# Kernel tuning notes

Measured on AMD Instinct MI355X. Metric: run time of the kernel, lower is better.

## Reference

```python
import jax, jax.numpy as jnp
import numpy as np

NLAT = 192  # octahedral O96-class grid


def _lons(nlat):
    half = [20 + 4 * i for i in range(nlat // 2)]
    return half + half[::-1]


def _dft_matrix(nlat, mmax):
    # Truncated per-ring real-DFT basis (torch.fft.rfft convention, 'forward' 1/n norm).
    # Ring j has nlon_j points; frequencies beyond its Nyquist (m > nlon_j//2) are zero.
    lons = _lons(nlat)
    max_nlon = max(lons)
    D = np.zeros((nlat, max_nlon, mmax), dtype=np.complex64)
    for j, n in enumerate(lons):
        keep = min(mmax, n // 2 + 1)
        k = np.arange(n)[:, None]
        m = np.arange(keep)[None, :]
        D[j, :n, :keep] = np.exp(-2j * np.pi * k * m / n) / n
    return D


def _legendre_weights(nlat, lmax, mmax):
    # Orthonormalized associated Legendre P_l^m at Gaussian latitudes (north->south),
    # with Gaussian quadrature weights and the 2*pi longitude factor folded in.
    xg, wg = np.polynomial.legendre.leggauss(nlat)
    x = xg[::-1].copy()
    w = wg[::-1].copy()
    s = np.sqrt(1.0 - x * x)
    leg = np.zeros((lmax, mmax, nlat))
    pmm = np.full(nlat, 1.0 / np.sqrt(4.0 * np.pi))
    for m in range(mmax):
        if m > 0:
            pmm = -np.sqrt((2 * m + 1) / (2.0 * m)) * s * pmm
        if m < lmax:
            leg[m, m] = pmm
        if m + 1 < lmax:
            leg[m + 1, m] = np.sqrt(2 * m + 3.0) * x * pmm
        for l in range(m + 2, lmax):
            a = np.sqrt((4.0 * l * l - 1.0) / (l * l - m * m))
            bb = np.sqrt(((2.0 * l + 1.0) * (l - 1 + m) * (l - 1 - m)) / ((2.0 * l - 3.0) * (l * l - m * m)))
            leg[l, m] = a * x * leg[l - 1, m] - bb * leg[l - 2, m]
    leg = 2.0 * np.pi * leg * w[None, None, :]
    return leg.astype(np.float32)


def setup_inputs() -> dict:
    key = jax.random.key(0)
    nlat = NLAT
    lmax = mmax = nlat // 2
    n_points = sum(_lons(nlat))  # 40320 for nlat=192
    data = jax.random.normal(key, (4, 1, 1, n_points, 100), dtype=jnp.float32)
    dft = jnp.asarray(_dft_matrix(nlat, mmax))
    leg = jnp.asarray(_legendre_weights(nlat, lmax, mmax))
    return {"data": data, "dft": dft, "leg": leg}


def reference(data, dft, leg):
    b, t, e, p, v = data.shape
    nlat, max_nlon, mmax = dft.shape
    lmax = leg.shape[0]
    lons = _lons(nlat)
    # static scatter map: flattened ragged rings -> [nlat, max_nlon] padded layout
    flat_idx = np.concatenate([j * max_nlon + np.arange(n) for j, n in enumerate(lons)])
    x = jnp.transpose(data, (0, 1, 2, 4, 3)).reshape(-1, p)  # [(b t e v), p]
    B = x.shape[0]
    x_pad = jnp.zeros((B, nlat * max_nlon), x.dtype).at[:, flat_idx].set(x)
    x_pad = x_pad.reshape(B, nlat, max_nlon)
    # ragged per-ring truncated real DFT, then associated-Legendre contraction
    f_hat = jnp.einsum('bjn,jnm->bjm', x_pad, dft)        # [B, nlat, mmax] complex
    coeffs = jnp.einsum('bjm,lmj->blm', f_hat, leg)       # [B, lmax, mmax] complex
    coeffs = coeffs.reshape(b, t, e, v, lmax, mmax)
    return jnp.transpose(coeffs, (0, 1, 2, 4, 5, 3))      # [b, t, e, yF, xF, v]
```

## Files before the change

### kernel.cpp

```cpp
#include <hip/hip_runtime.h>

#define NLAT 192
#define NPTS 40320
#define MMAX 96
#define LMAX 96
#define NV   100
#define MAXN 400
#define NB   400

typedef __attribute__((ext_vector_type(8))) _Float16 half8v;
typedef __attribute__((ext_vector_type(4))) float f32x4;

#define FSTR 40

static __device__ __forceinline__ float bits2f(unsigned int b) {
    union { unsigned int i; float f; } v; v.i = b; return v.f;
}
static __device__ __forceinline__ unsigned int f2bf(float f) {
    union { float f; unsigned int i; } v; v.f = f;
    return (v.i + 0x7FFFu + ((v.i >> 16) & 1u)) >> 16;
}
static __device__ __forceinline__ unsigned short f2h(float f) {
    _Float16 h = (_Float16)f;
    union { _Float16 h; unsigned short s; } u; u.h = h; return u.s;
}
static __device__ __forceinline__ float h2f(unsigned short s) {
    union { _Float16 h; unsigned short s; } u; u.s = s; return (float)u.h;
}

static __device__ __forceinline__ int Ssum(int n) {
    int q = n >> 3, r = n & 7; return 4 * q * (q - 1) + q * r;
}
static __device__ __forceinline__ int atoffk(int j) {
    if (j < 96) return 32 * (Ssum(j + 12) - 4);
    return 32 * (672 + 676 - Ssum(204 - j));
}
static __device__ __forceinline__ int kpad_of(int j) {
    return 32 * ((j < 96 ? (j + 12) : (203 - j)) >> 3);
}

__global__ __launch_bounds__(256) void leg_conv_kernel(
    const float* __restrict__ leg,
    unsigned short* __restrict__ legh,
    unsigned short* __restrict__ legl)
{
    int idx = blockIdx.x * 256 + threadIdx.x;
    if (idx >= 96 * 96 * 192) return;
    int j = idx % 192;
    int lm = idx / 192;
    int m = lm % 96, l = lm / 96;
    float v = leg[idx];
    unsigned short h = f2h(v);
    unsigned short lo = f2h(v - h2f(h));
    size_t o = ((size_t)m * 96 + l) * 192 + j;
    legh[o] = h;
    legl[o] = lo;
}

__global__ __launch_bounds__(256) void dft_transpose_kernel(
    const unsigned int* __restrict__ dftw,
    unsigned short* __restrict__ At)
{
    const int j = blockIdx.x;
    const int kpad = kpad_of(j);
    const int t = blockIdx.y;
    const int k0 = t * 32;
    if (k0 >= kpad) return;
    const int n = j < 96 ? 20 + 4 * j : 400 - 4 * (j - 96);
    unsigned short* abase = At + (size_t)atoffk(j) * 192 + (size_t)t * 6144;
    const int tid = threadIdx.x;
#pragma unroll
    for (int s = 0; s < 3; ++s) {
        int slot = s * 256 + tid;
        int row = slot % 192;
        int ch  = slot / 192;
        int m = row < 96 ? row : row - 96;
        bool isIm = row >= 96;
        const unsigned int* dp = dftw + ((size_t)j * MAXN + k0 + ch * 8) * 96 + m;
        unsigned short o[8];
#pragma unroll
        for (int i = 0; i < 8; ++i) {
            int k = k0 + ch * 8 + i;
            unsigned int v = (k < n) ? dp[(size_t)i * 96] : 0u;
            float f = isIm ? bits2f(v & 0xFFFF0000u) : bits2f(v << 16);
            o[i] = f2h(f);
        }
        uint4 pk;
        pk.x = (unsigned int)o[0] | ((unsigned int)o[1] << 16);
        pk.y = (unsigned int)o[2] | ((unsigned int)o[3] << 16);
        pk.z = (unsigned int)o[4] | ((unsigned int)o[5] << 16);
        pk.w = (unsigned int)o[6] | ((unsigned int)o[7] << 16);
        *(uint4*)(abase + (size_t)row * 32 + ch * 8) = pk;
    }
}

__global__ __launch_bounds__(256) void dft_mfma_kernel(
    const float* __restrict__ data,
    const unsigned short* __restrict__ At,
    unsigned short* __restrict__ fh,
    int c0, int cn)
{
    __shared__ unsigned short Xh_lds[2][64 * 32];
    __shared__ unsigned short Xl_lds[2][64 * 32];

    const int id  = blockIdx.x;
    const int j   = id % 192;
    const int bt  = id / 192;
    const int tid = threadIdx.x;
    const int w   = tid >> 6;
    const int l   = tid & 63;
    const int lr  = l & 15;
    const int kg  = l >> 4;
    const int kgp = kg ^ ((lr >> 1) & 3);

    int n, start;
    if (j < 96) { n = 20 + 4 * j; start = 2 * j * j + 18 * j; }
    else { int jj = j - 96; n = 400 - 4 * jj; start = 20160 + 402 * jj - 2 * jj * jj; }
    const int nsteps = kpad_of(j) >> 5;
    const unsigned short* abase = At + (size_t)atoffk(j) * 192;

    const int Bb = c0 + bt * 50;
    const int bb = Bb / NV;
    const int vb = Bb % NV;
    const float* dbase = data + (size_t)bb * NPTS * NV + vb;

    const int xc  = tid >> 2;
    const int xch = tid & 3;
    const int xpc = xch ^ ((xc >> 1) & 3);

    f32x4 acc[3][4];
#pragma unroll
    for (int i = 0; i < 3; ++i)
#pragma unroll
        for (int nt = 0; nt < 4; ++nt) acc[i][nt] = (f32x4){0.f, 0.f, 0.f, 0.f};

    float xv[8];

    {
        const float* sp = dbase + (size_t)(start + xch * 8) * NV + xc;
#pragma unroll
        for (int i = 0; i < 8; ++i) {
            int k = xch * 8 + i;
            xv[i] = (xc < 50 && k < n) ? sp[(size_t)i * NV] : 0.f;
        }
        unsigned int hw[4], lw[4];
#pragma unroll
        for (int t2 = 0; t2 < 4; ++t2) {
            unsigned short h0 = f2h(xv[2 * t2]), h1 = f2h(xv[2 * t2 + 1]);
            unsigned short l0 = f2h(xv[2 * t2] - h2f(h0));
            unsigned short l1 = f2h(xv[2 * t2 + 1] - h2f(h1));
            hw[t2] = (unsigned int)h0 | ((unsigned int)h1 << 16);
            lw[t2] = (unsigned int)l0 | ((unsigned int)l1 << 16);
        }
        *(uint4*)&Xh_lds[0][xc * 32 + xpc * 8] = (uint4){hw[0], hw[1], hw[2], hw[3]};
        *(uint4*)&Xl_lds[0][xc * 32 + xpc * 8] = (uint4){lw[0], lw[1], lw[2], lw[3]};
        __syncthreads();
    }

    int buf = 0;
    for (int t = 0; t < nsteps; ++t) {
        const int nb = buf ^ 1;
        const bool pf = (t + 1 < nsteps);

        if (pf) {
            const float* sp = dbase + (size_t)(start + (t + 1) * 32 + xch * 8) * NV + xc;
#pragma unroll
            for (int i = 0; i < 8; ++i) {
                int k = (t + 1) * 32 + xch * 8 + i;
                xv[i] = (xc < 50 && k < n) ? sp[(size_t)i * NV] : 0.f;
            }
        }

        const half8v* av = (const half8v*)(abase + (size_t)t * 6144);
        half8v a0 = av[((3 * w + 0) * 16 + lr) * 4 + kg];
        half8v a1 = av[((3 * w + 1) * 16 + lr) * 4 + kg];
        half8v a2 = av[((3 * w + 2) * 16 + lr) * 4 + kg];

#pragma unroll
        for (int nt = 0; nt < 4; ++nt) {
            half8v bh = *(const half8v*)&Xh_lds[buf][(nt * 16 + lr) * 32 + kgp * 8];
            half8v bl = *(const half8v*)&Xl_lds[buf][(nt * 16 + lr) * 32 + kgp * 8];
            acc[0][nt] = __builtin_amdgcn_mfma_f32_16x16x32_f16(a0, bh, acc[0][nt], 0, 0, 0);
            acc[1][nt] = __builtin_amdgcn_mfma_f32_16x16x32_f16(a1, bh, acc[1][nt], 0, 0, 0);
            acc[2][nt] = __builtin_amdgcn_mfma_f32_16x16x32_f16(a2, bh, acc[2][nt], 0, 0, 0);
            acc[0][nt] = __builtin_amdgcn_mfma_f32_16x16x32_f16(a0, bl, acc[0][nt], 0, 0, 0);
            acc[1][nt] = __builtin_amdgcn_mfma_f32_16x16x32_f16(a1, bl, acc[1][nt], 0, 0, 0);
            acc[2][nt] = __builtin_amdgcn_mfma_f32_16x16x32_f16(a2, bl, acc[2][nt], 0, 0, 0);
        }

        if (pf) {
            unsigned int hw[4], lw[4];
#pragma unroll
            for (int t2 = 0; t2 < 4; ++t2) {
                unsigned short h0 = f2h(xv[2 * t2]), h1 = f2h(xv[2 * t2 + 1]);
                unsigned short l0 = f2h(xv[2 * t2] - h2f(h0));
                unsigned short l1 = f2h(xv[2 * t2 + 1] - h2f(h1));
                hw[t2] = (unsigned int)h0 | ((unsigned int)h1 << 16);
                lw[t2] = (unsigned int)l0 | ((unsigned int)l1 << 16);
            }
            *(uint4*)&Xh_lds[nb][xc * 32 + xpc * 8] = (uint4){hw[0], hw[1], hw[2], hw[3]};
            *(uint4*)&Xl_lds[nb][xc * 32 + xpc * 8] = (uint4){lw[0], lw[1], lw[2], lw[3]};
        }
        __syncthreads();
        buf = nb;
    }

#pragma unroll
    for (int i = 0; i < 3; ++i)
#pragma unroll
        for (int nt = 0; nt < 4; ++nt) {
            int c = nt * 16 + lr;
            if (c < 50) {
                int Brel = bt * 50 + c;
                int mm0 = (3 * w + i) * 16 + kg * 4;
                unsigned short* oh = fh + ((size_t)j * 192 + mm0) * cn + Brel;
#pragma unroll
                for (int r = 0; r < 4; ++r)
                    oh[(size_t)r * cn] = f2h(acc[i][nt][r]);
            }
        }
}

__global__ __launch_bounds__(256) void leg_mfma_kernel(
    const unsigned short* __restrict__ legh,
    const unsigned short* __restrict__ legl,
    const unsigned short* __restrict__ fh,
    unsigned int* __restrict__ out,
    int c0, int cn)
{
    __shared__ unsigned short A_lds[2 * 96 * FSTR];
    __shared__ unsigned short F_lds[2 * 64 * FSTR];

    const int m   = blockIdx.x;
    const int bt  = blockIdx.y;
    const int tid = threadIdx.x;
    const int w   = tid >> 6;
    const int l   = tid & 63;
    const int lr  = l & 15;
    const int kg  = l >> 4;

    f32x4 acc[6][2];
#pragma unroll
    for (int lt = 0; lt < 6; ++lt)
#pragma unroll
        for (int pl = 0; pl < 2; ++pl) acc[lt][pl] = (f32x4){0.f, 0.f, 0.f, 0.f};

    const unsigned int* lh32 = (const unsigned int*)legh;
    const unsigned int* ll32 = (const unsigned int*)legl;
    const unsigned int* f32p = (const unsigned int*)fh;

    for (int j0 = 0; j0 < NLAT; j0 += 32) {
        __syncthreads();

#pragma unroll
        for (int s = 0; s < 12; ++s) {
            const int hl = (s >= 6) ? 1 : 0;
            int rem = tid + 256 * s - 1536 * hl;
            int lrow = rem >> 4;
            int ku = rem & 15;
            const unsigned int* src = hl ? ll32 : lh32;
            unsigned int v = src[((size_t)m * 96 + lrow) * 96 + (j0 >> 1) + ku];
            ((unsigned int*)A_lds)[(size_t)hl * 96 * (FSTR / 2) + lrow * (FSTR / 2) + ku] = v;
        }

#pragma unroll
        for (int s = 0; s < 7; ++s) {
            int q = tid + 256 * s;
            if (q < 1600) {
                int u  = q % 25;
                int r2 = q / 25;
                int jj = r2 & 31;
                int pl = r2 >> 5;
                unsigned int v = f32p[((size_t)(j0 + jj) * 192 + m + 96 * pl) * (cn >> 1)
                                      + bt * 25 + u];
                size_t base = ((size_t)pl * 64 + 2 * u) * FSTR + jj;
                F_lds[base]        = (unsigned short)(v & 0xFFFFu);
                F_lds[base + FSTR] = (unsigned short)(v >> 16);
            }
        }
        __syncthreads();

        half8v fF[2];
#pragma unroll
        for (int pl = 0; pl < 2; ++pl)
            fF[pl] = *(const half8v*)&F_lds[((size_t)pl * 64 + w * 16 + lr) * FSTR + kg * 8];
#pragma unroll
        for (int lt = 0; lt < 6; ++lt) {
            half8v ah = *(const half8v*)&A_lds[(size_t)(0 * 96 + lt * 16 + lr) * FSTR + kg * 8];
            half8v al = *(const half8v*)&A_lds[(size_t)(1 * 96 + lt * 16 + lr) * FSTR + kg * 8];
#pragma unroll
            for (int pl = 0; pl < 2; ++pl) {
                acc[lt][pl] = __builtin_amdgcn_mfma_f32_16x16x32_f16(ah, fF[pl], acc[lt][pl], 0, 0, 0);
                acc[lt][pl] = __builtin_amdgcn_mfma_f32_16x16x32_f16(al, fF[pl], acc[lt][pl], 0, 0, 0);
            }
        }
    }

    int c = w * 16 + lr;
    if (c < 50) {
        int B = c0 + bt * 50 + c;
        int bb = B / NV, vv = B % NV;
#pragma unroll
        for (int lt = 0; lt < 6; ++lt) {
#pragma unroll
            for (int r = 0; r < 4; ++r) {
                int ll = lt * 16 + kg * 4 + r;
                out[(((size_t)bb * LMAX + ll) * MMAX + m) * NV + vv] =
                    f2bf(acc[lt][0][r]) | (f2bf(acc[lt][1][r]) << 16);
            }
        }
    }
}

extern "C" void kernel_launch(void* const* d_in, const int* in_sizes, int n_in,
                              void* d_out, int out_size, void* d_ws, size_t ws_size,
                              hipStream_t stream) {
    if (n_in != 3) return;

    const float* data = (const float*)d_in[0];
    const unsigned int* dftw = (const unsigned int*)d_in[1];
    const float* leg  = (const float*)d_in[2];
    unsigned int* out = (unsigned int*)d_out;

    const size_t LEGN = (size_t)96 * 96 * 192;
    const size_t LEGB = 2 * LEGN * sizeof(unsigned short);
    const size_t ATN  = (size_t)43008 * 192;
    const size_t ATB  = ATN * sizeof(unsigned short);
    const size_t rowb = (size_t)192 * 192 * sizeof(unsigned short);
    if (ws_size < LEGB + ATB + 50 * rowb) return;

    unsigned short* legh = (unsigned short*)d_ws;
    unsigned short* legl = legh + LEGN;
    unsigned short* At   = legl + LEGN;

    size_t maxrows = (ws_size - LEGB - ATB) / rowb;
    int chunk = (int)((maxrows / 50) * 50);
    if (chunk > NB) chunk = NB;

    leg_conv_kernel<<<dim3((96 * 96 * 192 + 255) / 256), dim3(256), 0, stream>>>(
        leg, legh, legl);
    dft_transpose_kernel<<<dim3(192, 13), dim3(256), 0, stream>>>(dftw, At);

    for (int c0 = 0; c0 < NB; c0 += chunk) {
        int cn = NB - c0 < chunk ? NB - c0 : chunk;
        unsigned short* fh = At + ATN;

        int nbt = cn / 50;
        dim3 g1(192 * nbt);
        dft_mfma_kernel<<<g1, dim3(256), 0, stream>>>(data, At, fh, c0, cn);
        dim3 g2(96, nbt);
        leg_mfma_kernel<<<g2, dim3(256), 0, stream>>>(legh, legl, fh, out, c0, cn);
    }
}
```

Measured before the change: 90.93 us.

## Drop LDS staging; load MFMA operands directly from global into registers

Both the DFT and Legendre MFMA kernels stop staging operands through shared memory. Each wave now loads its B fragments (data columns, f_hat values) and its Legendre A fragments straight from global memory into registers, and the DFT kernel splits fp32 into hi/lo halves in registers. This removes the LDS writes, LDS reads and __syncthreads barriers. In exchange, every wave redundantly fetches the same data, and the global loads are strided scalar 2-byte or 4-byte accesses that rely on the caches.

```diff
diff --git a/kernel.cpp b/kernel.cpp
--- a/kernel.cpp
+++ b/kernel.cpp
@@ -11,8 +11,6 @@
 typedef __attribute__((ext_vector_type(8))) _Float16 half8v;
 typedef __attribute__((ext_vector_type(4))) float f32x4;
 
-#define FSTR 40
-
 static __device__ __forceinline__ float bits2f(unsigned int b) {
     union { unsigned int i; float f; } v; v.i = b; return v.f;
 }
@@ -21,11 +19,17 @@
     return (v.i + 0x7FFFu + ((v.i >> 16) & 1u)) >> 16;
 }
 static __device__ __forceinline__ unsigned short f2h(float f) {
-    _Float16 h = (_Float16)f;
-    union { _Float16 h; unsigned short s; } u; u.h = h; return u.s;
+    union { _Float16 h; unsigned short s; } u; u.h = (_Float16)f; return u.s;
 }
 static __device__ __forceinline__ float h2f(unsigned short s) {
     union { _Float16 h; unsigned short s; } u; u.s = s; return (float)u.h;
+}
+static __device__ __forceinline__ void split2(float a, float b,
+                                              unsigned int& hw, unsigned int& lw) {
+    unsigned short h0 = f2h(a), h1 = f2h(b);
+    unsigned short l0 = f2h(a - h2f(h0)), l1 = f2h(b - h2f(h1));
+    hw = (unsigned int)h0 | ((unsigned int)h1 << 16);
+    lw = (unsigned int)l0 | ((unsigned int)l1 << 16);
 }
 
 static __device__ __forceinline__ int Ssum(int n) {
@@ -100,9 +104,6 @@
     unsigned short* __restrict__ fh,
     int c0, int cn)
 {
-    __shared__ unsigned short Xh_lds[2][64 * 32];
-    __shared__ unsigned short Xl_lds[2][64 * 32];
-
     const int id  = blockIdx.x;
     const int j   = id % 192;
     const int bt  = id / 192;
@@ -111,75 +112,69 @@
     const int l   = tid & 63;
     const int lr  = l & 15;
     const int kg  = l >> 4;
-    const int kgp = kg ^ ((lr >> 1) & 3);
 
     int n, start;
     if (j < 96) { n = 20 + 4 * j; start = 2 * j * j + 18 * j; }
     else { int jj = j - 96; n = 400 - 4 * jj; start = 20160 + 402 * jj - 2 * jj * jj; }
     const int nsteps = kpad_of(j) >> 5;
-    const unsigned short* abase = At + (size_t)atoffk(j) * 192;
+    const half8v* avbase = (const half8v*)(At + (size_t)atoffk(j) * 192);
 
     const int Bb = c0 + bt * 50;
     const int bb = Bb / NV;
     const int vb = Bb % NV;
     const float* dbase = data + (size_t)bb * NPTS * NV + vb;
 
-    const int xc  = tid >> 2;
-    const int xch = tid & 3;
-    const int xpc = xch ^ ((xc >> 1) & 3);
-
     f32x4 acc[3][4];
 #pragma unroll
     for (int i = 0; i < 3; ++i)
 #pragma unroll
         for (int nt = 0; nt < 4; ++nt) acc[i][nt] = (f32x4){0.f, 0.f, 0.f, 0.f};
 
-    float xv[8];
-
-    {
-        const float* sp = dbase + (size_t)(start + xch * 8) * NV + xc;
+    float xf[4][8];
+#pragma unroll
+    for (int nt = 0; nt < 4; ++nt) {
+        int c = nt * 16 + lr;
+        const float* sp = dbase + (size_t)(start + kg * 8) * NV + c;
 #pragma unroll
         for (int i = 0; i < 8; ++i) {
-            int k = xch * 8 + i;
-            xv[i] = (xc < 50 && k < n) ? sp[(size_t)i * NV] : 0.f;
-        }
-        unsigned int hw[4], lw[4];
-#pragma unroll
-        for (int t2 = 0; t2 < 4; ++t2) {
-            unsigned short h0 = f2h(xv[2 * t2]), h1 = f2h(xv[2 * t2 + 1]);
-            unsigned short l0 = f2h(xv[2 * t2] - h2f(h0));
-            unsigned short l1 = f2h(xv[2 * t2 + 1] - h2f(h1));
-            hw[t2] = (unsigned int)h0 | ((unsigned int)h1 << 16);
-            lw[t2] = (unsigned int)l0 | ((unsigned int)l1 << 16);
-        }
-        *(uint4*)&Xh_lds[0][xc * 32 + xpc * 8] = (uint4){hw[0], hw[1], hw[2], hw[3]};
-        *(uint4*)&Xl_lds[0][xc * 32 + xpc * 8] = (uint4){lw[0], lw[1], lw[2], lw[3]};
-        __syncthreads();
-    }
-
-    int buf = 0;
+            int k = kg * 8 + i;
+            xf[nt][i] = (c < 50 && k < n) ? sp[(size_t)i * NV] : 0.f;
+        }
+    }
+
     for (int t = 0; t < nsteps; ++t) {
-        const int nb = buf ^ 1;
-        const bool pf = (t + 1 < nsteps);
-
-        if (pf) {
-            const float* sp = dbase + (size_t)(start + (t + 1) * 32 + xch * 8) * NV + xc;
-#pragma unroll
-            for (int i = 0; i < 8; ++i) {
-                int k = (t + 1) * 32 + xch * 8 + i;
-                xv[i] = (xc < 50 && k < n) ? sp[(size_t)i * NV] : 0.f;
-            }
-        }
-
-        const half8v* av = (const half8v*)(abase + (size_t)t * 6144);
+        const half8v* av = avbase + (size_t)t * 768;
         half8v a0 = av[((3 * w + 0) * 16 + lr) * 4 + kg];
         half8v a1 = av[((3 * w + 1) * 16 + lr) * 4 + kg];
         half8v a2 = av[((3 * w + 2) * 16 + lr) * 4 + kg];
 
+        unsigned int BH[4][4], BL[4][4];
+#pragma unroll
+        for (int nt = 0; nt < 4; ++nt)
+#pragma unroll
+            for (int q = 0; q < 4; ++q)
+                split2(xf[nt][2 * q], xf[nt][2 * q + 1], BH[nt][q], BL[nt][q]);
+
+        if (t + 1 < nsteps) {
+            int kb = (t + 1) * 32 + kg * 8;
+#pragma unroll
+            for (int nt = 0; nt < 4; ++nt) {
+                int c = nt * 16 + lr;
+                const float* sp = dbase + (size_t)(start + kb) * NV + c;
+#pragma unroll
+                for (int i = 0; i < 8; ++i) {
+                    int k = kb + i;
+                    xf[nt][i] = (c < 50 && k < n) ? sp[(size_t)i * NV] : 0.f;
+                }
+            }
+        }
+
 #pragma unroll
         for (int nt = 0; nt < 4; ++nt) {
-            half8v bh = *(const half8v*)&Xh_lds[buf][(nt * 16 + lr) * 32 + kgp * 8];
-            half8v bl = *(const half8v*)&Xl_lds[buf][(nt * 16 + lr) * 32 + kgp * 8];
+            union { uint4 u; half8v h; } ub, ul2;
+            ub.u = (uint4){BH[nt][0], BH[nt][1], BH[nt][2], BH[nt][3]};
+            ul2.u = (uint4){BL[nt][0], BL[nt][1], BL[nt][2], BL[nt][3]};
+            half8v bh = ub.h, bl = ul2.h;
             acc[0][nt] = __builtin_amdgcn_mfma_f32_16x16x32_f16(a0, bh, acc[0][nt], 0, 0, 0);
             acc[1][nt] = __builtin_amdgcn_mfma_f32_16x16x32_f16(a1, bh, acc[1][nt], 0, 0, 0);
             acc[2][nt] = __builtin_amdgcn_mfma_f32_16x16x32_f16(a2, bh, acc[2][nt], 0, 0, 0);
@@ -187,22 +182,6 @@
             acc[1][nt] = __builtin_amdgcn_mfma_f32_16x16x32_f16(a1, bl, acc[1][nt], 0, 0, 0);
             acc[2][nt] = __builtin_amdgcn_mfma_f32_16x16x32_f16(a2, bl, acc[2][nt], 0, 0, 0);
         }
-
-        if (pf) {
-            unsigned int hw[4], lw[4];
-#pragma unroll
-            for (int t2 = 0; t2 < 4; ++t2) {
-                unsigned short h0 = f2h(xv[2 * t2]), h1 = f2h(xv[2 * t2 + 1]);
-                unsigned short l0 = f2h(xv[2 * t2] - h2f(h0));
-                unsigned short l1 = f2h(xv[2 * t2 + 1] - h2f(h1));
-                hw[t2] = (unsigned int)h0 | ((unsigned int)h1 << 16);
-                lw[t2] = (unsigned int)l0 | ((unsigned int)l1 << 16);
-            }
-            *(uint4*)&Xh_lds[nb][xc * 32 + xpc * 8] = (uint4){hw[0], hw[1], hw[2], hw[3]};
-            *(uint4*)&Xl_lds[nb][xc * 32 + xpc * 8] = (uint4){lw[0], lw[1], lw[2], lw[3]};
-        }
-        __syncthreads();
-        buf = nb;
     }
 
 #pragma unroll
@@ -228,9 +207,6 @@
     unsigned int* __restrict__ out,
     int c0, int cn)
 {
-    __shared__ unsigned short A_lds[2 * 96 * FSTR];
-    __shared__ unsigned short F_lds[2 * 64 * FSTR];
-
     const int m   = blockIdx.x;
     const int bt  = blockIdx.y;
     const int tid = threadIdx.x;
@@ -239,65 +215,43 @@
     const int lr  = l & 15;
     const int kg  = l >> 4;
 
+    const int c  = w * 16 + lr;
+    const bool cok = c < 50;
+    const int col = bt * 50 + (cok ? c : 0);
+
     f32x4 acc[6][2];
 #pragma unroll
     for (int lt = 0; lt < 6; ++lt)
 #pragma unroll
         for (int pl = 0; pl < 2; ++pl) acc[lt][pl] = (f32x4){0.f, 0.f, 0.f, 0.f};
 
-    const unsigned int* lh32 = (const unsigned int*)legh;
-    const unsigned int* ll32 = (const unsigned int*)legl;
-    const unsigned int* f32p = (const unsigned int*)fh;
-
     for (int j0 = 0; j0 < NLAT; j0 += 32) {
-        __syncthreads();
-
-#pragma unroll
-        for (int s = 0; s < 12; ++s) {
-            const int hl = (s >= 6) ? 1 : 0;
-            int rem = tid + 256 * s - 1536 * hl;
-            int lrow = rem >> 4;
-            int ku = rem & 15;
-            const unsigned int* src = hl ? ll32 : lh32;
-            unsigned int v = src[((size_t)m * 96 + lrow) * 96 + (j0 >> 1) + ku];
-            ((unsigned int*)A_lds)[(size_t)hl * 96 * (FSTR / 2) + lrow * (FSTR / 2) + ku] = v;
-        }
-
-#pragma unroll
-        for (int s = 0; s < 7; ++s) {
-            int q = tid + 256 * s;
-            if (q < 1600) {
-                int u  = q % 25;
-                int r2 = q / 25;
-                int jj = r2 & 31;
-                int pl = r2 >> 5;
-                unsigned int v = f32p[((size_t)(j0 + jj) * 192 + m + 96 * pl) * (cn >> 1)
-                                      + bt * 25 + u];
-                size_t base = ((size_t)pl * 64 + 2 * u) * FSTR + jj;
-                F_lds[base]        = (unsigned short)(v & 0xFFFFu);
-                F_lds[base + FSTR] = (unsigned short)(v >> 16);
+        half8v ah[6], al[6];
+#pragma unroll
+        for (int lt = 0; lt < 6; ++lt) {
+            size_t o = ((size_t)m * 96 + lt * 16 + lr) * 192 + j0 + kg * 8;
+            ah[lt] = *(const half8v*)&legh[o];
+            al[lt] = *(const half8v*)&legl[o];
+        }
+        half8v fF[2];
+#pragma unroll
+        for (int pl = 0; pl < 2; ++pl) {
+            union { half8v h; unsigned short s[8]; } uf;
+#pragma unroll
+            for (int i = 0; i < 8; ++i)
+                uf.s[i] = fh[((size_t)(j0 + kg * 8 + i) * 192 + m + 96 * pl) * cn + col];
+            fF[pl] = uf.h;
+        }
+#pragma unroll
+        for (int lt = 0; lt < 6; ++lt)
+#pragma unroll
+            for (int pl = 0; pl < 2; ++pl) {
+                acc[lt][pl] = __builtin_amdgcn_mfma_f32_16x16x32_f16(ah[lt], fF[pl], acc[lt][pl], 0, 0, 0);
+                acc[lt][pl] = __builtin_amdgcn_mfma_f32_16x16x32_f16(al[lt], fF[pl], acc[lt][pl], 0, 0, 0);
             }
-        }
-        __syncthreads();
-
-        half8v fF[2];
-#pragma unroll
-        for (int pl = 0; pl < 2; ++pl)
-            fF[pl] = *(const half8v*)&F_lds[((size_t)pl * 64 + w * 16 + lr) * FSTR + kg * 8];
-#pragma unroll
-        for (int lt = 0; lt < 6; ++lt) {
-            half8v ah = *(const half8v*)&A_lds[(size_t)(0 * 96 + lt * 16 + lr) * FSTR + kg * 8];
-            half8v al = *(const half8v*)&A_lds[(size_t)(1 * 96 + lt * 16 + lr) * FSTR + kg * 8];
-#pragma unroll
-            for (int pl = 0; pl < 2; ++pl) {
-                acc[lt][pl] = __builtin_amdgcn_mfma_f32_16x16x32_f16(ah, fF[pl], acc[lt][pl], 0, 0, 0);
-                acc[lt][pl] = __builtin_amdgcn_mfma_f32_16x16x32_f16(al, fF[pl], acc[lt][pl], 0, 0, 0);
-            }
-        }
-    }
-
-    int c = w * 16 + lr;
-    if (c < 50) {
+    }
+
+    if (cok) {
         int B = c0 + bt * 50 + c;
         int bb = B / NV, vv = B % NV;
 #pragma unroll
```

After: 96.15 us. 5.7% more time.
